# Performance work log

Hardware: AMD Instinct MI355X
Metric: run time of the kernel (lower is better)

The kernel has to match this reference:

```python
import jax, jax.numpy as jnp
import numpy as np

N_NODES = 100000
N_EDGES = 1600000
IN_CH = 128
OUT_CH = 64
H1 = 4 * OUT_CH  # 256
H2 = 2 * OUT_CH  # 128


def setup_inputs() -> dict:
    key = jax.random.key(0)
    ks = jax.random.split(key, 6)
    x = jax.random.normal(ks[0], (N_NODES, IN_CH), dtype=jnp.float32)
    edge_index = jax.random.randint(ks[1], (2, N_EDGES), 0, N_NODES, dtype=jnp.int64)
    # Glorot-style init for the three GCNConv weight matrices
    W1 = jax.random.normal(ks[2], (IN_CH, H1), dtype=jnp.float32) / np.sqrt(IN_CH)
    W2 = jax.random.normal(ks[3], (H1, H2), dtype=jnp.float32) / np.sqrt(H1)
    W3 = jax.random.normal(ks[4], (H2, OUT_CH), dtype=jnp.float32) / np.sqrt(H2)
    b1 = jnp.zeros((H1,), jnp.float32)
    b2 = jnp.zeros((H2,), jnp.float32)
    b3 = jnp.zeros((OUT_CH,), jnp.float32)
    return {"x": x, "edge_index": edge_index, "W1": W1, "b1": b1,
            "W2": W2, "b2": b2, "W3": W3, "b3": b3}


def reference(x, edge_index, W1, b1, W2, b2, W3, b3):
    N = x.shape[0]
    # GCNConv semantics (PyG defaults): add self-loops, symmetric D^-1/2 A D^-1/2 norm.
    loops = jnp.arange(N, dtype=edge_index.dtype)
    src = jnp.concatenate([edge_index[0], loops])  # message sources
    dst = jnp.concatenate([edge_index[1], loops])  # aggregation targets
    deg = jax.ops.segment_sum(jnp.ones_like(dst, x.dtype), dst, num_segments=N)
    dinv = jax.lax.rsqrt(jnp.maximum(deg, 1.0))  # deg >= 1 due to self-loops
    norm = dinv[src] * dinv[dst]  # [E+N] per-edge normalization

    def gcn(h, W, b):
        h = h @ W                                   # dense transform first
        msg = h[src] * norm[:, None]                # gather + normalize
        return jax.ops.segment_sum(msg, dst, num_segments=N) + b

    h = gcn(x, W1, b1)
    h = jax.nn.relu(gcn(h, W2, b2))
    return gcn(h, W3, b3)
```

## Files before the change

### kernel.cpp

```cpp
#include <hip/hip_runtime.h>
#include <cstddef>
#include <cstdint>

#define NND 100000
#define NED 1600000
#define NEP (NED + NND)

typedef short v8s __attribute__((ext_vector_type(8)));
typedef float v4f __attribute__((ext_vector_type(4)));

__device__ __forceinline__ uint32_t f32_to_bf16_rne(float x) {
    uint32_t u = __builtin_bit_cast(uint32_t, x);
    return (u + 0x7fffu + ((u >> 16) & 1u)) >> 16;
}
__device__ __forceinline__ float bf16bits_to_f32(uint32_t b) {
    return __builtin_bit_cast(float, b << 16);
}

__global__ void k_detect(const long long* __restrict__ ei, int* __restrict__ flag) {
    __shared__ int ok;
    if (threadIdx.x == 0) ok = 1;
    __syncthreads();
    for (int i = threadIdx.x; i < 2048; i += blockDim.x) {
        long long v = ei[i];
        if (v < 0 || v >= NND) ok = 0;
    }
    __syncthreads();
    if (threadIdx.x == 0) *flag = ok;
}

__device__ __forceinline__ void load_edge(const void* ei, int is64, int e, int& src, int& dst) {
    if (e >= NED) { src = dst = e - NED; return; }
    if (is64) {
        const long long* p = (const long long*)ei;
        src = (int)p[e];
        dst = (int)p[NED + e];
    } else {
        const int* p = (const int*)ei;
        src = p[e];
        dst = p[NED + e];
    }
}

__global__ void k_deg(const void* __restrict__ ei, const int* __restrict__ flag,
                      int* __restrict__ deg) {
    int e = blockIdx.x * 256 + threadIdx.x;
    if (e >= NEP) return;
    int s, d;
    load_edge(ei, *flag, e, s, d);
    atomicAdd(&deg[d], 1);
}

__global__ void k_dinv(const int* __restrict__ deg, float* __restrict__ dinv) {
    int n = blockIdx.x * 256 + threadIdx.x;
    if (n >= NND) return;
    int d = deg[n];
    if (d < 1) d = 1;
    dinv[n] = 1.0f / sqrtf((float)d);
}

__global__ __launch_bounds__(1024) void k_scan1(const int* __restrict__ deg,
                                                int* __restrict__ row_off,
                                                int* __restrict__ bsum) {
    __shared__ int sh[1024];
    int i = blockIdx.x * 1024 + threadIdx.x;
    int v = (i < NND) ? deg[i] : 0;
    sh[threadIdx.x] = v;
    __syncthreads();
    for (int off = 1; off < 1024; off <<= 1) {
        int t = 0;
        if ((int)threadIdx.x >= off) t = sh[threadIdx.x - off];
        __syncthreads();
        sh[threadIdx.x] += t;
        __syncthreads();
    }
    if (i < NND) row_off[i] = sh[threadIdx.x] - v;
    if (threadIdx.x == 1023) bsum[blockIdx.x] = sh[1023];
}

__global__ void k_scan2(int* __restrict__ bsum, int nb) {
    __shared__ int sh[128];
    int t = threadIdx.x;
    int orig = (t < nb) ? bsum[t] : 0;
    sh[t] = orig;
    __syncthreads();
    for (int off = 1; off < 128; off <<= 1) {
        int v = 0;
        if (t >= off) v = sh[t - off];
        __syncthreads();
        sh[t] += v;
        __syncthreads();
    }
    if (t < nb) bsum[t] = sh[t] - orig;
}

__global__ void k_scan3(int* __restrict__ row_off, const int* __restrict__ bsum) {
    int i = blockIdx.x * 256 + threadIdx.x;
    if (i < NND) row_off[i] += bsum[i >> 10];
    if (i == 0) row_off[NND] = NEP;
}

__global__ void k_fill(const void* __restrict__ ei, const int* __restrict__ flag,
                       const int* __restrict__ row_off, int* __restrict__ cursor,
                       int* __restrict__ col) {
    int e = blockIdx.x * 256 + threadIdx.x;
    if (e >= NEP) return;
    int s, d;
    load_edge(ei, *flag, e, s, d);
    int pos = row_off[d] + atomicAdd(&cursor[d], 1);
    col[pos] = s;
}

__global__ void k_wcomb(const float* __restrict__ W1, const float* __restrict__ W2,
                        const float* __restrict__ b1, float* __restrict__ Wc,
                        float* __restrict__ bc) {
    const int j = threadIdx.x;
    const int i = blockIdx.x;
    const float* rowv = (i < 128) ? (W1 + (size_t)i * 256) : b1;
    float acc = 0.f;
    for (int k = 0; k < 256; ++k) acc = fmaf(rowv[k], W2[(size_t)k * 128 + j], acc);
    if (i < 128) Wc[(size_t)i * 128 + j] = acc;
    else bc[j] = acc;
}

__global__ void k_wprep(const float* __restrict__ W, unsigned short* __restrict__ wth,
                        unsigned short* __restrict__ wtl, int K, int N) {
    int i = blockIdx.x * 256 + threadIdx.x;
    if (i >= K * N) return;
    int k = i / N, n = i % N;
    float x = W[i];
    uint32_t hi = f32_to_bf16_rne(x);
    float resid = x - bf16bits_to_f32(hi);
    uint32_t lo = f32_to_bf16_rne(resid);
    wth[(size_t)n * K + k] = (unsigned short)hi;
    wtl[(size_t)n * K + k] = (unsigned short)lo;
}

template <int C, bool BIAS, bool RELU, bool OUT_SPLIT>
__global__ __launch_bounds__(C) void k_agg(const float* __restrict__ in, float* __restrict__ out,
                      const int* __restrict__ row_off, const int* __restrict__ col,
                      const float* __restrict__ dinv, const float* __restrict__ bias,
                      unsigned short* __restrict__ outh, unsigned short* __restrict__ outl) {
    constexpr int LPG = C / 4;
    constexpr int NG = 4;
    constexpr int MAXE = 256;
    __shared__ int sidx[MAXE];
    __shared__ float snrm[MAXE];
    __shared__ float4 red[NG][LPG];

    const int n = blockIdx.x;
    const int t = threadIdx.x;
    const int g = t / LPG;
    const int l = t % LPG;
    const int s = row_off[n], e = row_off[n + 1];
    const float4* __restrict__ in4 = (const float4*)in;

    float4 a0 = make_float4(0.f, 0.f, 0.f, 0.f);
    float4 a1 = make_float4(0.f, 0.f, 0.f, 0.f);
    float4 a2 = make_float4(0.f, 0.f, 0.f, 0.f);
    float4 a3 = make_float4(0.f, 0.f, 0.f, 0.f);

    for (int base = s; base < e; base += MAXE) {
        const int cnt = min(e - base, MAXE);
        for (int i = t; i < cnt; i += C) {
            int c = col[base + i];
            sidx[i] = c;
            snrm[i] = dinv[c];
        }
        __syncthreads();

        int k = g;
        for (; k + 3 * NG < cnt; k += 4 * NG) {
            int s0 = sidx[k];
            int s1 = sidx[k + NG];
            int s2 = sidx[k + 2 * NG];
            int s3 = sidx[k + 3 * NG];
            float d0 = snrm[k];
            float d1 = snrm[k + NG];
            float d2 = snrm[k + 2 * NG];
            float d3 = snrm[k + 3 * NG];
            float4 v0 = in4[(size_t)s0 * LPG + l];
            float4 v1 = in4[(size_t)s1 * LPG + l];
            float4 v2 = in4[(size_t)s2 * LPG + l];
            float4 v3 = in4[(size_t)s3 * LPG + l];
            a0.x = fmaf(d0, v0.x, a0.x); a0.y = fmaf(d0, v0.y, a0.y);
            a0.z = fmaf(d0, v0.z, a0.z); a0.w = fmaf(d0, v0.w, a0.w);
            a1.x = fmaf(d1, v1.x, a1.x); a1.y = fmaf(d1, v1.y, a1.y);
            a1.z = fmaf(d1, v1.z, a1.z); a1.w = fmaf(d1, v1.w, a1.w);
            a2.x = fmaf(d2, v2.x, a2.x); a2.y = fmaf(d2, v2.y, a2.y);
            a2.z = fmaf(d2, v2.z, a2.z); a2.w = fmaf(d2, v2.w, a2.w);
            a3.x = fmaf(d3, v3.x, a3.x); a3.y = fmaf(d3, v3.y, a3.y);
            a3.z = fmaf(d3, v3.z, a3.z); a3.w = fmaf(d3, v3.w, a3.w);
        }
        for (; k < cnt; k += NG) {
            int s0 = sidx[k];
            float d0 = snrm[k];
            float4 v0 = in4[(size_t)s0 * LPG + l];
            a0.x = fmaf(d0, v0.x, a0.x); a0.y = fmaf(d0, v0.y, a0.y);
            a0.z = fmaf(d0, v0.z, a0.z); a0.w = fmaf(d0, v0.w, a0.w);
        }
        __syncthreads();
    }

    a0.x += a1.x + a2.x + a3.x;
    a0.y += a1.y + a2.y + a3.y;
    a0.z += a1.z + a2.z + a3.z;
    a0.w += a1.w + a2.w + a3.w;
    red[g][l] = a0;
    __syncthreads();
    if (g == 0) {
        float4 r = red[0][l];
        float4 r1 = red[1][l];
        float4 r2 = red[2][l];
        float4 r3 = red[3][l];
        r.x += r1.x + r2.x + r3.x;
        r.y += r1.y + r2.y + r3.y;
        r.z += r1.z + r2.z + r3.z;
        r.w += r1.w + r2.w + r3.w;
        float dn = dinv[n];
        r.x *= dn; r.y *= dn; r.z *= dn; r.w *= dn;
        if constexpr (BIAS) {
            float4 bv = ((const float4*)bias)[l];
            r.x += bv.x; r.y += bv.y; r.z += bv.z; r.w += bv.w;
        }
        if constexpr (RELU) {
            r.x = fmaxf(r.x, 0.f); r.y = fmaxf(r.y, 0.f);
            r.z = fmaxf(r.z, 0.f); r.w = fmaxf(r.w, 0.f);
        }
        if constexpr (OUT_SPLIT) {
            uint32_t h0 = f32_to_bf16_rne(r.x), h1 = f32_to_bf16_rne(r.y);
            uint32_t h2 = f32_to_bf16_rne(r.z), h3 = f32_to_bf16_rne(r.w);
            uint32_t l0 = f32_to_bf16_rne(r.x - bf16bits_to_f32(h0));
            uint32_t l1 = f32_to_bf16_rne(r.y - bf16bits_to_f32(h1));
            uint32_t l2 = f32_to_bf16_rne(r.z - bf16bits_to_f32(h2));
            uint32_t l3 = f32_to_bf16_rne(r.w - bf16bits_to_f32(h3));
            uint2 oh = make_uint2(h0 | (h1 << 16), h2 | (h3 << 16));
            uint2 ol = make_uint2(l0 | (l1 << 16), l2 | (l3 << 16));
            *(uint2*)(outh + (size_t)n * C + l * 4) = oh;
            *(uint2*)(outl + (size_t)n * C + l * 4) = ol;
        } else {
            ((float4*)out)[(size_t)n * LPG + l] = r;
        }
    }
}

template <int K, int N, int WN, int WM, bool BIAS, bool OUT_SPLIT>
__global__ __launch_bounds__(WN * WM * 64, 3) void k_mgemm(
    const unsigned short* __restrict__ acth, const unsigned short* __restrict__ actl,
    const unsigned short* __restrict__ wth, const unsigned short* __restrict__ wtl,
    const float* __restrict__ bias, float* __restrict__ outf,
    unsigned short* __restrict__ outh, unsigned short* __restrict__ outl, int nrows)
{
    constexpr int BM = 64;
    constexpr int BK = 128;
    constexpr int NCH = K / BK;
    constexpr int KC = BK / 32;
    constexpr int KP = BK + 8;
    constexpr int NTW = N / (WN * 16);
    constexpr int RT = 4 / WM;
    constexpr int NTHR = WN * WM * 64;
    constexpr int CHUNKS = BM * BK / 8;

    __shared__ unsigned short sh[2][BM][KP];

    const int tid = threadIdx.x;
    const int lane = tid & 63;
    const int wave = tid >> 6;
    const int wn = wave % WN;
    const int wm = wave / WN;
    const int l15 = lane & 15;
    const int lq = lane >> 4;
    const int r0 = blockIdx.x * BM;
    const int ncol0 = wn * NTW * 16;

    v8s wh[NTW][K / 32], wl[NTW][K / 32];
#pragma unroll
    for (int nt = 0; nt < NTW; ++nt) {
        const size_t nrow = (size_t)(ncol0 + nt * 16 + l15) * K;
#pragma unroll
        for (int kk = 0; kk < K / 32; ++kk) {
            wh[nt][kk] = *(const v8s*)(wth + nrow + kk * 32 + lq * 8);
            wl[nt][kk] = *(const v8s*)(wtl + nrow + kk * 32 + lq * 8);
        }
    }

    v4f acc[RT][NTW];
#pragma unroll
    for (int rt = 0; rt < RT; ++rt)
#pragma unroll
        for (int nt = 0; nt < NTW; ++nt) acc[rt][nt] = (v4f){0.f, 0.f, 0.f, 0.f};

#pragma unroll
    for (int ch = 0; ch < NCH; ++ch) {
        if (ch) __syncthreads();
        for (int i = tid; i < 2 * CHUNKS; i += NTHR) {
            const int plane = i >= CHUNKS;
            const int j = plane ? i - CHUNKS : i;
            const int r = j / (BK / 8);
            const int c = (j % (BK / 8)) * 8;
            int gr = r0 + r;
            if (gr >= nrows) gr = nrows - 1;
            const unsigned short* src = (plane ? actl : acth) + (size_t)gr * K + ch * BK + c;
            *(v8s*)(&sh[plane][r][c]) = *(const v8s*)src;
        }
        __syncthreads();

#pragma unroll
        for (int kc = 0; kc < KC; ++kc) {
#pragma unroll
            for (int rt = 0; rt < RT; ++rt) {
                const int row = (wm * RT + rt) * 16 + l15;
                const v8s ah = *(const v8s*)(&sh[0][row][kc * 32 + lq * 8]);
                const v8s al = *(const v8s*)(&sh[1][row][kc * 32 + lq * 8]);
                const int kk = ch * KC + kc;
#pragma unroll
                for (int nt = 0; nt < NTW; ++nt) {
                    acc[rt][nt] = __builtin_amdgcn_mfma_f32_16x16x32_bf16(wh[nt][kk], ah, acc[rt][nt], 0, 0, 0);
                    acc[rt][nt] = __builtin_amdgcn_mfma_f32_16x16x32_bf16(wh[nt][kk], al, acc[rt][nt], 0, 0, 0);
                    acc[rt][nt] = __builtin_amdgcn_mfma_f32_16x16x32_bf16(wl[nt][kk], ah, acc[rt][nt], 0, 0, 0);
                }
            }
        }
    }

#pragma unroll
    for (int rt = 0; rt < RT; ++rt) {
        const int m = r0 + (wm * RT + rt) * 16 + l15;
        if (m >= nrows) continue;
#pragma unroll
        for (int nt = 0; nt < NTW; ++nt) {
            const int nc = ncol0 + nt * 16 + lq * 4;
            v4f v = acc[rt][nt];
            if constexpr (BIAS) {
                float4 bv = *(const float4*)(bias + nc);
                v[0] += bv.x; v[1] += bv.y; v[2] += bv.z; v[3] += bv.w;
            }
            if constexpr (OUT_SPLIT) {
                uint32_t h0 = f32_to_bf16_rne(v[0]), h1 = f32_to_bf16_rne(v[1]);
                uint32_t h2 = f32_to_bf16_rne(v[2]), h3 = f32_to_bf16_rne(v[3]);
                uint32_t l0 = f32_to_bf16_rne(v[0] - bf16bits_to_f32(h0));
                uint32_t l1 = f32_to_bf16_rne(v[1] - bf16bits_to_f32(h1));
                uint32_t l2 = f32_to_bf16_rne(v[2] - bf16bits_to_f32(h2));
                uint32_t l3 = f32_to_bf16_rne(v[3] - bf16bits_to_f32(h3));
                *(uint2*)(outh + (size_t)m * N + nc) = make_uint2(h0 | (h1 << 16), h2 | (h3 << 16));
                *(uint2*)(outl + (size_t)m * N + nc) = make_uint2(l0 | (l1 << 16), l2 | (l3 << 16));
            } else {
                *(float4*)(outf + (size_t)m * N + nc) = make_float4(v[0], v[1], v[2], v[3]);
            }
        }
    }
}

extern "C" void kernel_launch(void* const* d_in, const int* in_sizes, int n_in,
                              void* d_out, int out_size, void* d_ws, size_t ws_size,
                              hipStream_t stream) {
    const float* x = (const float*)d_in[0];
    const void* ei = d_in[1];
    const float* W1 = (const float*)d_in[2];
    const float* b1 = (const float*)d_in[3];
    const float* W2 = (const float*)d_in[4];
    const float* b2 = (const float*)d_in[5];
    const float* W3 = (const float*)d_in[6];
    const float* b3 = (const float*)d_in[7];
    float* out = (float*)d_out;

    char* ws = (char*)d_ws;
    size_t off = 0;
    auto alloc = [&](size_t bytes) -> void* {
        void* p = ws + off;
        off = (off + bytes + 255) & ~(size_t)255;
        return p;
    };

    int* flag = (int*)alloc(sizeof(int));
    int* deg = (int*)alloc((size_t)NND * 4);
    int* cursor = (int*)alloc((size_t)NND * 4);
    int* row_off = (int*)alloc((size_t)(NND + 1) * 4);
    int* bsum = (int*)alloc(512);
    float* dinv = (float*)alloc((size_t)NND * 4);
    int* col = (int*)alloc((size_t)NEP * 4);
    float* Wc = (float*)alloc((size_t)128 * 128 * 4);
    float* bc = (float*)alloc((size_t)128 * 4);
    unsigned short* wtCh = (unsigned short*)alloc((size_t)128 * 128 * 2);
    unsigned short* wtCl = (unsigned short*)alloc((size_t)128 * 128 * 2);
    unsigned short* wt3h = (unsigned short*)alloc((size_t)128 * 64 * 2);
    unsigned short* wt3l = (unsigned short*)alloc((size_t)128 * 64 * 2);
    unsigned short* AXh = (unsigned short*)alloc((size_t)NND * 128 * 2 * 2);
    unsigned short* AXl = AXh + (size_t)NND * 128;
    float* H2 = (float*)alloc((size_t)NND * 128 * 4);
    unsigned short* A2h = AXh;
    unsigned short* A2l = AXl;
    float* H3 = H2;

    hipMemsetAsync(deg, 0, (size_t)NND * 4, stream);
    hipMemsetAsync(cursor, 0, (size_t)NND * 4, stream);

    k_detect<<<1, 256, 0, stream>>>((const long long*)ei, flag);

    const int gE = (NEP + 255) / 256;
    const int gN = (NND + 255) / 256;
    k_deg<<<gE, 256, 0, stream>>>(ei, flag, deg);
    k_dinv<<<gN, 256, 0, stream>>>(deg, dinv);

    const int NB = (NND + 1023) / 1024;
    k_scan1<<<NB, 1024, 0, stream>>>(deg, row_off, bsum);
    k_scan2<<<1, 128, 0, stream>>>(bsum, NB);
    k_scan3<<<gN, 256, 0, stream>>>(row_off, bsum);

    k_fill<<<gE, 256, 0, stream>>>(ei, flag, row_off, cursor, col);

    k_wcomb<<<129, 128, 0, stream>>>(W1, W2, b1, Wc, bc);
    k_wprep<<<(128 * 128 + 255) / 256, 256, 0, stream>>>(Wc, wtCh, wtCl, 128, 128);
    k_wprep<<<(128 * 64 + 255) / 256, 256, 0, stream>>>(W3, wt3h, wt3l, 128, 64);

    const int gT = (NND + 63) / 64;

    k_agg<128, false, false, true><<<NND, 128, 0, stream>>>(x, nullptr, row_off, col, dinv, nullptr, AXh, AXl);
    k_mgemm<128, 128, 8, 1, true, false><<<gT, 512, 0, stream>>>(AXh, AXl, wtCh, wtCl, bc, H2, nullptr, nullptr, NND);

    k_agg<128, true, true, true><<<NND, 128, 0, stream>>>(H2, nullptr, row_off, col, dinv, b2, A2h, A2l);

    k_mgemm<128, 64, 4, 2, false, false><<<gT, 512, 0, stream>>>(A2h, A2l, wt3h, wt3l, nullptr, H3, nullptr, nullptr, NND);
    k_agg<64, true, false, false><<<NND, 64, 0, stream>>>(H3, out, row_off, col, dinv, b3, nullptr, nullptr);
}
```

Baseline: 543.7 us.

## Make aggregation kernels persistent with prefetch of next node's neighbor list

Replaces the one-block-per-node aggregation launch with a fixed grid of 4096 persistent blocks that loop over nodes in strides. Each block prefetches the next node's row offsets, column indices and norms into registers while it processes the current node. The C=64 layer now uses 128 threads, split as 8 edge groups. The dinv computation is folded into the first scan kernel, which removes one launch. The intent is to cut per-block launch and sync overhead and to hide index-load latency, at the cost of a fixed grid size and more register pressure.

```diff
diff --git a/kernel.cpp b/kernel.cpp
--- a/kernel.cpp
+++ b/kernel.cpp
@@ -51,20 +51,17 @@
     atomicAdd(&deg[d], 1);
 }
 
-__global__ void k_dinv(const int* __restrict__ deg, float* __restrict__ dinv) {
-    int n = blockIdx.x * 256 + threadIdx.x;
-    if (n >= NND) return;
-    int d = deg[n];
-    if (d < 1) d = 1;
-    dinv[n] = 1.0f / sqrtf((float)d);
-}
-
 __global__ __launch_bounds__(1024) void k_scan1(const int* __restrict__ deg,
                                                 int* __restrict__ row_off,
-                                                int* __restrict__ bsum) {
+                                                int* __restrict__ bsum,
+                                                float* __restrict__ dinv) {
     __shared__ int sh[1024];
     int i = blockIdx.x * 1024 + threadIdx.x;
     int v = (i < NND) ? deg[i] : 0;
+    if (i < NND) {
+        int d = v < 1 ? 1 : v;
+        dinv[i] = 1.0f / sqrtf((float)d);
+    }
     sh[threadIdx.x] = v;
     __syncthreads();
     for (int off = 1; off < 1024; off <<= 1) {
@@ -137,110 +134,139 @@
 }
 
 template <int C, bool BIAS, bool RELU, bool OUT_SPLIT>
-__global__ __launch_bounds__(C) void k_agg(const float* __restrict__ in, float* __restrict__ out,
-                      const int* __restrict__ row_off, const int* __restrict__ col,
-                      const float* __restrict__ dinv, const float* __restrict__ bias,
-                      unsigned short* __restrict__ outh, unsigned short* __restrict__ outl) {
+__global__ __launch_bounds__(128) void k_agg(
+    const float* __restrict__ in, float* __restrict__ out,
+    const int* __restrict__ row_off, const int* __restrict__ col,
+    const float* __restrict__ dinv, const float* __restrict__ bias,
+    unsigned short* __restrict__ outh, unsigned short* __restrict__ outl)
+{
     constexpr int LPG = C / 4;
-    constexpr int NG = 4;
-    constexpr int MAXE = 256;
+    constexpr int NG = 128 / LPG;
+    constexpr int MAXE = 128;
     __shared__ int sidx[MAXE];
     __shared__ float snrm[MAXE];
     __shared__ float4 red[NG][LPG];
 
-    const int n = blockIdx.x;
     const int t = threadIdx.x;
     const int g = t / LPG;
     const int l = t % LPG;
-    const int s = row_off[n], e = row_off[n + 1];
+    const int G = gridDim.x;
     const float4* __restrict__ in4 = (const float4*)in;
 
-    float4 a0 = make_float4(0.f, 0.f, 0.f, 0.f);
-    float4 a1 = make_float4(0.f, 0.f, 0.f, 0.f);
-    float4 a2 = make_float4(0.f, 0.f, 0.f, 0.f);
-    float4 a3 = make_float4(0.f, 0.f, 0.f, 0.f);
-
-    for (int base = s; base < e; base += MAXE) {
-        const int cnt = min(e - base, MAXE);
-        for (int i = t; i < cnt; i += C) {
-            int c = col[base + i];
-            sidx[i] = c;
-            snrm[i] = dinv[c];
-        }
-        __syncthreads();
-
+    int n = blockIdx.x;
+    if (n >= NND) return;
+    int s = row_off[n];
+    int e = row_off[n + 1];
+    float dn = dinv[n];
+    {
+        int cnt = e - s;
+        if (cnt > MAXE) cnt = MAXE;
+        int c = 0; float d = 0.f;
+        if (t < cnt) { c = col[s + t]; d = dinv[c]; }
+        sidx[t] = c; snrm[t] = d;
+    }
+    __syncthreads();
+
+    while (true) {
+        const int nn = n + G;
+        const bool havenext = (nn < NND);
+        int s2 = 0, e2 = 0, c2 = 0;
+        float d2 = 0.f, dn2 = 0.f;
+        if (havenext) {
+            s2 = row_off[nn];
+            e2 = row_off[nn + 1];
+            dn2 = dinv[nn];
+            int cnt2 = e2 - s2;
+            if (cnt2 > MAXE) cnt2 = MAXE;
+            if (t < cnt2) { c2 = col[s2 + t]; d2 = dinv[c2]; }
+        }
+
+        const int cnt = e - s;
+        const int scnt = cnt > MAXE ? MAXE : cnt;
+        float4 a0 = make_float4(0.f, 0.f, 0.f, 0.f);
+        float4 a1 = make_float4(0.f, 0.f, 0.f, 0.f);
+        float4 a2 = make_float4(0.f, 0.f, 0.f, 0.f);
+        float4 a3 = make_float4(0.f, 0.f, 0.f, 0.f);
         int k = g;
-        for (; k + 3 * NG < cnt; k += 4 * NG) {
+        for (; k + 3 * NG < scnt; k += 4 * NG) {
             int s0 = sidx[k];
             int s1 = sidx[k + NG];
-            int s2 = sidx[k + 2 * NG];
+            int ss2 = sidx[k + 2 * NG];
             int s3 = sidx[k + 3 * NG];
             float d0 = snrm[k];
-            float d1 = snrm[k + NG];
-            float d2 = snrm[k + 2 * NG];
-            float d3 = snrm[k + 3 * NG];
+            float dd1 = snrm[k + NG];
+            float dd2 = snrm[k + 2 * NG];
+            float dd3 = snrm[k + 3 * NG];
             float4 v0 = in4[(size_t)s0 * LPG + l];
             float4 v1 = in4[(size_t)s1 * LPG + l];
-            float4 v2 = in4[(size_t)s2 * LPG + l];
+            float4 v2 = in4[(size_t)ss2 * LPG + l];
             float4 v3 = in4[(size_t)s3 * LPG + l];
             a0.x = fmaf(d0, v0.x, a0.x); a0.y = fmaf(d0, v0.y, a0.y);
             a0.z = fmaf(d0, v0.z, a0.z); a0.w = fmaf(d0, v0.w, a0.w);
-            a1.x = fmaf(d1, v1.x, a1.x); a1.y = fmaf(d1, v1.y, a1.y);
-            a1.z = fmaf(d1, v1.z, a1.z); a1.w = fmaf(d1, v1.w, a1.w);
-            a2.x = fmaf(d2, v2.x, a2.x); a2.y = fmaf(d2, v2.y, a2.y);
-            a2.z = fmaf(d2, v2.z, a2.z); a2.w = fmaf(d2, v2.w, a2.w);
-            a3.x = fmaf(d3, v3.x, a3.x); a3.y = fmaf(d3, v3.y, a3.y);
-            a3.z = fmaf(d3, v3.z, a3.z); a3.w = fmaf(d3, v3.w, a3.w);
-        }
-        for (; k < cnt; k += NG) {
+            a1.x = fmaf(dd1, v1.x, a1.x); a1.y = fmaf(dd1, v1.y, a1.y);
+            a1.z = fmaf(dd1, v1.z, a1.z); a1.w = fmaf(dd1, v1.w, a1.w);
+            a2.x = fmaf(dd2, v2.x, a2.x); a2.y = fmaf(dd2, v2.y, a2.y);
+            a2.z = fmaf(dd2, v2.z, a2.z); a2.w = fmaf(dd2, v2.w, a2.w);
+            a3.x = fmaf(dd3, v3.x, a3.x); a3.y = fmaf(dd3, v3.y, a3.y);
+            a3.z = fmaf(dd3, v3.z, a3.z); a3.w = fmaf(dd3, v3.w, a3.w);
+        }
+        for (; k < scnt; k += NG) {
             int s0 = sidx[k];
             float d0 = snrm[k];
             float4 v0 = in4[(size_t)s0 * LPG + l];
             a0.x = fmaf(d0, v0.x, a0.x); a0.y = fmaf(d0, v0.y, a0.y);
             a0.z = fmaf(d0, v0.z, a0.z); a0.w = fmaf(d0, v0.w, a0.w);
         }
-        __syncthreads();
-    }
-
-    a0.x += a1.x + a2.x + a3.x;
-    a0.y += a1.y + a2.y + a3.y;
-    a0.z += a1.z + a2.z + a3.z;
-    a0.w += a1.w + a2.w + a3.w;
-    red[g][l] = a0;
-    __syncthreads();
-    if (g == 0) {
-        float4 r = red[0][l];
-        float4 r1 = red[1][l];
-        float4 r2 = red[2][l];
-        float4 r3 = red[3][l];
-        r.x += r1.x + r2.x + r3.x;
-        r.y += r1.y + r2.y + r3.y;
-        r.z += r1.z + r2.z + r3.z;
-        r.w += r1.w + r2.w + r3.w;
-        float dn = dinv[n];
-        r.x *= dn; r.y *= dn; r.z *= dn; r.w *= dn;
-        if constexpr (BIAS) {
-            float4 bv = ((const float4*)bias)[l];
-            r.x += bv.x; r.y += bv.y; r.z += bv.z; r.w += bv.w;
-        }
-        if constexpr (RELU) {
-            r.x = fmaxf(r.x, 0.f); r.y = fmaxf(r.y, 0.f);
-            r.z = fmaxf(r.z, 0.f); r.w = fmaxf(r.w, 0.f);
-        }
-        if constexpr (OUT_SPLIT) {
-            uint32_t h0 = f32_to_bf16_rne(r.x), h1 = f32_to_bf16_rne(r.y);
-            uint32_t h2 = f32_to_bf16_rne(r.z), h3 = f32_to_bf16_rne(r.w);
-            uint32_t l0 = f32_to_bf16_rne(r.x - bf16bits_to_f32(h0));
-            uint32_t l1 = f32_to_bf16_rne(r.y - bf16bits_to_f32(h1));
-            uint32_t l2 = f32_to_bf16_rne(r.z - bf16bits_to_f32(h2));
-            uint32_t l3 = f32_to_bf16_rne(r.w - bf16bits_to_f32(h3));
-            uint2 oh = make_uint2(h0 | (h1 << 16), h2 | (h3 << 16));
-            uint2 ol = make_uint2(l0 | (l1 << 16), l2 | (l3 << 16));
-            *(uint2*)(outh + (size_t)n * C + l * 4) = oh;
-            *(uint2*)(outl + (size_t)n * C + l * 4) = ol;
-        } else {
-            ((float4*)out)[(size_t)n * LPG + l] = r;
-        }
+        for (int kk = MAXE + g; kk < cnt; kk += NG) {
+            int c0 = col[s + kk];
+            float d0 = dinv[c0];
+            float4 v0 = in4[(size_t)c0 * LPG + l];
+            a0.x = fmaf(d0, v0.x, a0.x); a0.y = fmaf(d0, v0.y, a0.y);
+            a0.z = fmaf(d0, v0.z, a0.z); a0.w = fmaf(d0, v0.w, a0.w);
+        }
+
+        a0.x += a1.x + a2.x + a3.x;
+        a0.y += a1.y + a2.y + a3.y;
+        a0.z += a1.z + a2.z + a3.z;
+        a0.w += a1.w + a2.w + a3.w;
+        red[g][l] = a0;
+        __syncthreads();
+
+        if (g == 0) {
+            float4 r = red[0][l];
+#pragma unroll
+            for (int q = 1; q < NG; ++q) {
+                float4 rq = red[q][l];
+                r.x += rq.x; r.y += rq.y; r.z += rq.z; r.w += rq.w;
+            }
+            r.x *= dn; r.y *= dn; r.z *= dn; r.w *= dn;
+            if constexpr (BIAS) {
+                float4 bv = ((const float4*)bias)[l];
+                r.x += bv.x; r.y += bv.y; r.z += bv.z; r.w += bv.w;
+            }
+            if constexpr (RELU) {
+                r.x = fmaxf(r.x, 0.f); r.y = fmaxf(r.y, 0.f);
+                r.z = fmaxf(r.z, 0.f); r.w = fmaxf(r.w, 0.f);
+            }
+            if constexpr (OUT_SPLIT) {
+                uint32_t h0 = f32_to_bf16_rne(r.x), h1 = f32_to_bf16_rne(r.y);
+                uint32_t h2 = f32_to_bf16_rne(r.z), h3 = f32_to_bf16_rne(r.w);
+                uint32_t l0 = f32_to_bf16_rne(r.x - bf16bits_to_f32(h0));
+                uint32_t l1 = f32_to_bf16_rne(r.y - bf16bits_to_f32(h1));
+                uint32_t l2 = f32_to_bf16_rne(r.z - bf16bits_to_f32(h2));
+                uint32_t l3 = f32_to_bf16_rne(r.w - bf16bits_to_f32(h3));
+                *(uint2*)(outh + (size_t)n * C + l * 4) = make_uint2(h0 | (h1 << 16), h2 | (h3 << 16));
+                *(uint2*)(outl + (size_t)n * C + l * 4) = make_uint2(l0 | (l1 << 16), l2 | (l3 << 16));
+            } else {
+                ((float4*)out)[(size_t)n * LPG + l] = r;
+            }
+        }
+
+        if (!havenext) break;
+        sidx[t] = c2;
+        snrm[t] = d2;
+        n = nn; s = s2; e = e2; dn = dn2;
+        __syncthreads();
     }
 }
 
@@ -400,10 +426,9 @@
     const int gE = (NEP + 255) / 256;
     const int gN = (NND + 255) / 256;
     k_deg<<<gE, 256, 0, stream>>>(ei, flag, deg);
-    k_dinv<<<gN, 256, 0, stream>>>(deg, dinv);
 
     const int NB = (NND + 1023) / 1024;
-    k_scan1<<<NB, 1024, 0, stream>>>(deg, row_off, bsum);
+    k_scan1<<<NB, 1024, 0, stream>>>(deg, row_off, bsum, dinv);
     k_scan2<<<1, 128, 0, stream>>>(bsum, NB);
     k_scan3<<<gN, 256, 0, stream>>>(row_off, bsum);
 
@@ -414,12 +439,13 @@
     k_wprep<<<(128 * 64 + 255) / 256, 256, 0, stream>>>(W3, wt3h, wt3l, 128, 64);
 
     const int gT = (NND + 63) / 64;
-
-    k_agg<128, false, false, true><<<NND, 128, 0, stream>>>(x, nullptr, row_off, col, dinv, nullptr, AXh, AXl);
+    const int GA = 4096;
+
+    k_agg<128, false, false, true><<<GA, 128, 0, stream>>>(x, nullptr, row_off, col, dinv, nullptr, AXh, AXl);
     k_mgemm<128, 128, 8, 1, true, false><<<gT, 512, 0, stream>>>(AXh, AXl, wtCh, wtCl, bc, H2, nullptr, nullptr, NND);
 
-    k_agg<128, true, true, true><<<NND, 128, 0, stream>>>(H2, nullptr, row_off, col, dinv, b2, A2h, A2l);
+    k_agg<128, true, true, true><<<GA, 128, 0, stream>>>(H2, nullptr, row_off, col, dinv, b2, A2h, A2l);
 
     k_mgemm<128, 64, 4, 2, false, false><<<gT, 512, 0, stream>>>(A2h, A2l, wt3h, wt3l, nullptr, H3, nullptr, nullptr, NND);
-    k_agg<64, true, false, false><<<NND, 64, 0, stream>>>(H3, out, row_off, col, dinv, b3, nullptr, nullptr);
-}
+    k_agg<64, true, false, false><<<GA, 128, 0, stream>>>(H3, out, row_off, col, dinv, b3, nullptr, nullptr);
+}
```

After: 605.5 us. 11.4% more time.
